# Kernel tuning notes

Measured on AMD Instinct MI355X. Metric: run time of the kernel, lower is better.

The kernel has to match this reference:

```python
import jax, jax.numpy as jnp
import numpy as np
import math

B, S, D, H, L = 4, 2048, 512, 8, 2
HD = D // H
NG = (3, 4, 5)
V = 30000          # n_gram_vocab_size
BASE = 31          # rolling hash base
NPATCH = 16
PLEN = S // NPATCH


def _ln(x, w, b, eps):
    m = x.mean(-1, keepdims=True)
    v = ((x - m) ** 2).mean(-1, keepdims=True)
    return (x - m) * jax.lax.rsqrt(v + eps) * w + b


def setup_inputs() -> dict:
    key = jax.random.key(0)
    ks = jax.random.split(key, 16)

    def nrm(i, shape, std=0.02):
        return jax.random.normal(ks[i], shape, dtype=jnp.float32) * std

    return {
        "byte_seq": jax.random.randint(ks[0], (B, S), 0, 256, dtype=jnp.int32),
        "patch_boundaries": jnp.arange(NPATCH + 1, dtype=jnp.int32) * PLEN,
        "byte_emb": nrm(1, (256, D), 1.0 / math.sqrt(D)),
        "ng_emb": nrm(2, (len(NG), V, D)),
        "tl_qkv_w": nrm(3, (L, 3 * D, D)),
        "tl_qkv_b": jnp.zeros((L, 3 * D), jnp.float32),
        "tl_out_w": nrm(4, (L, D, D)),
        "tl_out_b": jnp.zeros((L, D), jnp.float32),
        "tl_ln1_w": jnp.ones((L, D), jnp.float32),
        "tl_ln1_b": jnp.zeros((L, D), jnp.float32),
        "tl_ln2_w": jnp.ones((L, D), jnp.float32),
        "tl_ln2_b": jnp.zeros((L, D), jnp.float32),
        "tl_ff1_w": nrm(5, (L, 4 * D, D)),
        "tl_ff1_b": jnp.zeros((L, 4 * D), jnp.float32),
        "tl_ff2_w": nrm(6, (L, D, 4 * D)),
        "tl_ff2_b": jnp.zeros((L, D), jnp.float32),
        "ca_qkv_w": nrm(7, (3 * D, D)),
        "ca_qkv_b": jnp.zeros((3 * D,), jnp.float32),
        "ca_out_w": nrm(8, (D, D)),
        "ca_out_b": jnp.zeros((D,), jnp.float32),
        "ca_ln_w": jnp.ones((D,), jnp.float32),
        "ca_ln_b": jnp.zeros((D,), jnp.float32),
        "norm_w": jnp.ones((D,), jnp.float32),
        "norm_b": jnp.zeros((D,), jnp.float32),
    }


def _forward(byte_seq, patch_boundaries, byte_emb, ng_emb,
             tl_qkv_w, tl_qkv_b, tl_out_w, tl_out_b,
             tl_ln1_w, tl_ln1_b, tl_ln2_w, tl_ln2_b,
             tl_ff1_w, tl_ff1_b, tl_ff2_w, tl_ff2_b,
             ca_qkv_w, ca_qkv_b, ca_out_w, ca_out_b, ca_ln_w, ca_ln_b,
             norm_w, norm_b):
    x = byte_emb[byte_seq]                                  # [B,S,D]

    # n-gram rolling hash == polynomial hash mod V; computed in parallel
    # as windowed dot products with modular base powers (exact same values
    # as the sequential rolling-update loop in the torch code).
    ng_scale = 1.0 / (len(NG) + 1)
    for idx, n in enumerate(NG):
        powers = jnp.array([pow(BASE, n - 1 - i, V) for i in range(n)],
                           dtype=byte_seq.dtype)
        windows = jnp.stack([byte_seq[:, j:S - n + 1 + j] for j in range(n)],
                            axis=-1)                        # [B,S-n+1,n]
        h = (windows * powers).sum(-1) % V                   # [B,S-n+1]
        x = x.at[:, n - 1:].add(ng_emb[idx][h] * ng_scale)

    scale = 1.0 / math.sqrt(HD)
    neg = jnp.where(jnp.triu(jnp.ones((S, S), dtype=bool), 1),
                    -jnp.inf, 0.0).astype(x.dtype)           # causal additive mask

    # post-norm TransformerEncoderLayer (relu activation, dropout=0/eval)
    for l in range(L):
        qkv = x @ tl_qkv_w[l].T + tl_qkv_b[l]                # [B,S,3D]
        q, k, v = jnp.split(qkv, 3, axis=-1)
        q = q.reshape(B, S, H, HD).transpose(0, 2, 1, 3)
        k = k.reshape(B, S, H, HD).transpose(0, 2, 1, 3)
        v = v.reshape(B, S, H, HD).transpose(0, 2, 1, 3)
        scores = jnp.einsum('bhqd,bhkd->bhqk', q, k) * scale + neg
        a = jax.nn.softmax(scores, axis=-1)
        o = jnp.einsum('bhqk,bhkd->bhqd', a, v).transpose(0, 2, 1, 3).reshape(B, S, D)
        o = o @ tl_out_w[l].T + tl_out_b[l]
        x = _ln(x + o, tl_ln1_w[l], tl_ln1_b[l], 1e-5)
        ff = jax.nn.relu(x @ tl_ff1_w[l].T + tl_ff1_b[l]) @ tl_ff2_w[l].T + tl_ff2_b[l]
        x = _ln(x + ff, tl_ln2_w[l], tl_ln2_b[l], 1e-5)

    # uniform patch boundaries -> vectorized patch cross-attention
    npatch = patch_boundaries.shape[0] - 1
    plen = S // npatch
    xp = x.reshape(B, npatch, plen, D)
    query = xp.mean(axis=2)                                  # [B,P,D]
    qn = _ln(query, ca_ln_w, ca_ln_b, 1e-6)
    kvn = _ln(xp, ca_ln_w, ca_ln_b, 1e-6)
    wq, wk, wv = jnp.split(ca_qkv_w, 3, axis=0)
    bq, bk, bv = jnp.split(ca_qkv_b, 3)
    q = (qn @ wq.T + bq).reshape(B, npatch, H, HD)
    k = (kvn @ wk.T + bk).reshape(B, npatch, plen, H, HD)
    v = (kvn @ wv.T + bv).reshape(B, npatch, plen, H, HD)
    s = jnp.einsum('bphd,bplhd->bphl', q, k) * scale
    a = jax.nn.softmax(s, axis=-1)
    o = jnp.einsum('bphl,bplhd->bphd', a, v).reshape(B, npatch, D)
    patches = query + (o @ ca_out_w.T + ca_out_b)

    return _ln(x, norm_w, norm_b, 1e-6), _ln(patches, norm_w, norm_b, 1e-6)


def reference(byte_seq, patch_boundaries, byte_emb, ng_emb,
              tl_qkv_w, tl_qkv_b, tl_out_w, tl_out_b,
              tl_ln1_w, tl_ln1_b, tl_ln2_w, tl_ln2_b,
              tl_ff1_w, tl_ff1_b, tl_ff2_w, tl_ff2_b,
              ca_qkv_w, ca_qkv_b, ca_out_w, ca_out_b, ca_ln_w, ca_ln_b,
              norm_w, norm_b):
    return _forward(byte_seq, patch_boundaries, byte_emb, ng_emb,
                    tl_qkv_w, tl_qkv_b, tl_out_w, tl_out_b,
                    tl_ln1_w, tl_ln1_b, tl_ln2_w, tl_ln2_b,
                    tl_ff1_w, tl_ff1_b, tl_ff2_w, tl_ff2_b,
                    ca_qkv_w, ca_qkv_b, ca_out_w, ca_out_b, ca_ln_w, ca_ln_b,
                    norm_w, norm_b)
```

## Files before the change

kernel.cpp:

```cpp
#include <hip/hip_runtime.h>
#include <hip/hip_bf16.h>

#define B_ 4
#define S_ 2048
#define D_ 512
#define H_ 8
#define HD_ 64
#define L_ 2
#define V_ 30000
#define NPATCH_ 16
#define PLEN_ 128

typedef short bf16x8 __attribute__((ext_vector_type(8)));
typedef float f32x4 __attribute__((ext_vector_type(4)));

__device__ __forceinline__ unsigned short f2bf(float f) {
    unsigned u = __float_as_uint(f);
    return (unsigned short)((u + 0x7FFFu + ((u >> 16) & 1u)) >> 16);
}
__device__ __forceinline__ float bf2f(unsigned short u) {
    return __uint_as_float(((unsigned int)u) << 16);
}

#define C0_ (2*1536*512/4)
#define C1_ (2*512*512/4)
#define C2_ (2*2048*512/4)
#define C3_ (2*512*2048/4)
#define C4_ (1024*512/4)
__global__ __launch_bounds__(256) void cast5_kernel(
    const float* __restrict__ s0, const float* __restrict__ s1,
    const float* __restrict__ s2, const float* __restrict__ s3,
    const float* __restrict__ s4,
    unsigned short* __restrict__ d0, unsigned short* __restrict__ d1,
    unsigned short* __restrict__ d2, unsigned short* __restrict__ d3,
    unsigned short* __restrict__ d4)
{
    int i = blockIdx.x * 256 + threadIdx.x;
    const float* s; unsigned short* d;
    if      (i < C0_)                  { s = s0; d = d0; }
    else if ((i -= C0_) < C1_)         { s = s1; d = d1; }
    else if ((i -= C1_) < C2_)         { s = s2; d = d2; }
    else if ((i -= C2_) < C3_)         { s = s3; d = d3; }
    else if ((i -= C3_) < C4_)         { s = s4; d = d4; }
    else return;
    const float4 v = *reinterpret_cast<const float4*>(s + (size_t)i * 4);
    ushort4 o;
    o.x = f2bf(v.x); o.y = f2bf(v.y); o.z = f2bf(v.z); o.w = f2bf(v.w);
    *reinterpret_cast<ushort4*>(d + (size_t)i * 4) = o;
}

__global__ __launch_bounds__(128) void embed_ngram_kernel(
    const int* __restrict__ bytes, const float* __restrict__ byte_emb,
    const float* __restrict__ ng_emb, float* __restrict__ x,
    unsigned short* __restrict__ xb)
{
    const int bs = blockIdx.x;
    const int s  = bs % S_;
    const int b  = bs / S_;
    const int d  = threadIdx.x * 4;
    const int* brow = bytes + (size_t)b * S_;

    const int c = brow[s];
    float4 v = *reinterpret_cast<const float4*>(byte_emb + (size_t)c * D_ + d);

    if (s >= 2) {
        int h = (brow[s-2]*961 + brow[s-1]*31 + brow[s]) % V_;
        const float4 g = *reinterpret_cast<const float4*>(ng_emb + ((size_t)0*V_ + h)*D_ + d);
        v.x += 0.25f*g.x; v.y += 0.25f*g.y; v.z += 0.25f*g.z; v.w += 0.25f*g.w;
    }
    if (s >= 3) {
        int h = (brow[s-3]*29791 + brow[s-2]*961 + brow[s-1]*31 + brow[s]) % V_;
        const float4 g = *reinterpret_cast<const float4*>(ng_emb + ((size_t)1*V_ + h)*D_ + d);
        v.x += 0.25f*g.x; v.y += 0.25f*g.y; v.z += 0.25f*g.z; v.w += 0.25f*g.w;
    }
    if (s >= 4) {
        int h = (brow[s-4]*23521 + brow[s-3]*29791 + brow[s-2]*961 + brow[s-1]*31 + brow[s]) % V_;
        const float4 g = *reinterpret_cast<const float4*>(ng_emb + ((size_t)2*V_ + h)*D_ + d);
        v.x += 0.25f*g.x; v.y += 0.25f*g.y; v.z += 0.25f*g.z; v.w += 0.25f*g.w;
    }
    *reinterpret_cast<float4*>(x + (size_t)bs * D_ + d) = v;
    ushort4 o;
    o.x = f2bf(v.x); o.y = f2bf(v.y); o.z = f2bf(v.z); o.w = f2bf(v.w);
    *reinterpret_cast<ushort4*>(xb + (size_t)bs * D_ + d) = o;
}

template<int DO_RELU, int BF16OUT, int BN, int VT, int RESID>
__global__ __launch_bounds__(256) void mgemm_kernel(
    const unsigned short* __restrict__ Xb, const unsigned short* __restrict__ Wb,
    const float* __restrict__ bias, void* __restrict__ Yout,
    unsigned short* __restrict__ vtb, const float* __restrict__ resid,
    int M, int N, int K)
{
    constexpr int NT  = BN / 32;
    constexpr int NLB = BN / 32;
    __shared__ unsigned short As[128*64];
    __shared__ unsigned short Bs[BN*64];

    const int t    = threadIdx.x;
    const int lane = t & 63;
    const int w    = t >> 6;

    const int nwg = gridDim.x * gridDim.y;
    const int bid = blockIdx.y * gridDim.x + blockIdx.x;
    const int swz = (bid & 7) * (nwg >> 3) + (bid >> 3);
    const int bx  = swz % gridDim.x, by = swz / gridDim.x;

    const int bm   = by * 128, bn = bx * BN;
    const int l15  = lane & 15, lg = lane >> 4;
    const int wr   = w >> 1, wc = w & 1;

    int srow[4], scol[4];
#pragma unroll
    for (int i = 0; i < 4; ++i) {
        const int off = w*1024 + i*4096 + lane*16;
        srow[i] = off >> 7;
        scol[i] = ((off >> 4) & 7) ^ (srow[i] & 7);
    }

    f32x4 acc[4][NT];
#pragma unroll
    for (int mt = 0; mt < 4; ++mt)
#pragma unroll
        for (int nt = 0; nt < NT; ++nt) acc[mt][nt] = (f32x4){0.f,0.f,0.f,0.f};

    for (int kt = 0; kt < K; kt += 64) {
#pragma unroll
        for (int i = 0; i < 4; ++i) {
            const unsigned short* gA = Xb + (size_t)(bm + srow[i]) * K + kt + scol[i]*8;
            __builtin_amdgcn_global_load_lds(
                (const __attribute__((address_space(1))) void*)gA,
                (__attribute__((address_space(3))) void*)&As[w*512 + i*2048], 16, 0, 0);
        }
#pragma unroll
        for (int i = 0; i < NLB; ++i) {
            const unsigned short* gB = Wb + (size_t)(bn + srow[i]) * K + kt + scol[i]*8;
            __builtin_amdgcn_global_load_lds(
                (const __attribute__((address_space(1))) void*)gB,
                (__attribute__((address_space(3))) void*)&Bs[w*512 + i*2048], 16, 0, 0);
        }
        __syncthreads();

#pragma unroll
        for (int ks = 0; ks < 2; ++ks) {
            const int c16 = (ks*4 + lg) ^ (l15 & 7);
            bf16x8 a[4], b[NT];
#pragma unroll
            for (int mt = 0; mt < 4; ++mt)
                a[mt] = *reinterpret_cast<const bf16x8*>(&As[(wr*64 + mt*16 + l15)*64 + c16*8]);
#pragma unroll
            for (int nt = 0; nt < NT; ++nt)
                b[nt] = *reinterpret_cast<const bf16x8*>(&Bs[(wc*(BN/2) + nt*16 + l15)*64 + c16*8]);
#pragma unroll
            for (int mt = 0; mt < 4; ++mt)
#pragma unroll
                for (int nt = 0; nt < NT; ++nt)
                    acc[mt][nt] = __builtin_amdgcn_mfma_f32_16x16x32_bf16(
                        a[mt], b[nt], acc[mt][nt], 0, 0, 0);
        }
        __syncthreads();
    }

    float bv[NT];
#pragma unroll
    for (int nt = 0; nt < NT; ++nt) bv[nt] = bias[bn + wc*(BN/2) + nt*16 + l15];

#pragma unroll
    for (int mt = 0; mt < 4; ++mt) {
#pragma unroll
        for (int nt = 0; nt < NT; ++nt) {
            const int n = bn + wc*(BN/2) + nt*16 + l15;
#pragma unroll
            for (int r = 0; r < 4; ++r) {
                const int m = bm + wr*64 + mt*16 + 4*lg + r;
                float v = acc[mt][nt][r] + bv[nt];
                if (DO_RELU) v = fmaxf(v, 0.f);
                if (RESID) v += resid[(size_t)m * N + n];
                if constexpr (VT) {
                    if (n < 1024)
                        ((unsigned short*)Yout)[(size_t)m * 1024 + n] = f2bf(v);
                    else
                        vtb[((size_t)(m >> 11) * 512 + (n - 1024)) * 2048 + (m & 2047)] = f2bf(v);
                } else if constexpr (BF16OUT) {
                    ((unsigned short*)Yout)[(size_t)m * N + n] = f2bf(v);
                } else {
                    ((float*)Yout)[(size_t)m * N + n] = v;
                }
            }
        }
    }
}

__global__ __launch_bounds__(256) void attn_mfma_kernel(
    const unsigned short* __restrict__ qkvb, const unsigned short* __restrict__ vtb,
    unsigned short* __restrict__ ob)
{
    __shared__ unsigned short Ks[128*72];
    __shared__ unsigned short Vt[64*136];
    __shared__ unsigned short Plds[4*16*136];

    const int t    = threadIdx.x;
    const int lane = t & 63;
    const int w    = t >> 6;
    const int qp   = blockIdx.x;
    const int bh   = blockIdx.y;
    const int h    = bh & 7;
    const int b    = bh >> 3;

    const unsigned short* base = qkvb + (size_t)b * S_ * 1024;
    const int l15 = lane & 15, lg = lane >> 4;
    const int skey = t >> 1;
    const int sd0  = (t & 1) * 32;
    const int sdv  = t >> 2;
    const int skc  = (t & 3) * 32;
    const unsigned short* vbase = vtb + ((size_t)b * 512 + h*64 + sdv) * 2048;
    unsigned short* pw_base = Plds + w*16*136;
    const int pxor = ((l15 >> 3) & 1) << 1;

    bf16x8 kr0, kr1, kr2, kr3, vr0, vr1, vr2, vr3;
#define LOADREG(KT) { \
        const unsigned short* pk_ = base + (size_t)((KT) + skey) * 1024 + 512 + h*64 + sd0; \
        kr0 = *reinterpret_cast<const bf16x8*>(pk_);       \
        kr1 = *reinterpret_cast<const bf16x8*>(pk_ + 8);   \
        kr2 = *reinterpret_cast<const bf16x8*>(pk_ + 16);  \
        kr3 = *reinterpret_cast<const bf16x8*>(pk_ + 24);  \
        const unsigned short* pv_ = vbase + (KT) + skc;    \
        vr0 = *reinterpret_cast<const bf16x8*>(pv_);       \
        vr1 = *reinterpret_cast<const bf16x8*>(pv_ + 8);   \
        vr2 = *reinterpret_cast<const bf16x8*>(pv_ + 16);  \
        vr3 = *reinterpret_cast<const bf16x8*>(pv_ + 24); }

    LOADREG(0);

#pragma unroll
    for (int half = 0; half < 2; ++half) {
        const int qb  = half ? (31 - qp) : qp;
        const int q0w = qb * 64 + w * 16;

        bf16x8 qf0, qf1;
        {
            const unsigned short* qr = base + (size_t)(q0w + l15) * 1024 + h*64 + lg*8;
            qf0 = *reinterpret_cast<const bf16x8*>(qr);
            qf1 = *reinterpret_cast<const bf16x8*>(qr + 32);
        }

        f32x4 oacc[4];
#pragma unroll
        for (int i = 0; i < 4; ++i) oacc[i] = (f32x4){0.f,0.f,0.f,0.f};
        float mrow[4] = {-INFINITY,-INFINITY,-INFINITY,-INFINITY};
        float lrow[4] = {0.f,0.f,0.f,0.f};

        const int ntiles = (qb + 2) >> 1;
        for (int tile = 0; tile < ntiles; ++tile) {
            const int kt = tile * 128;
            __syncthreads();
            *reinterpret_cast<bf16x8*>(&Ks[skey*72 + sd0])      = kr0;
            *reinterpret_cast<bf16x8*>(&Ks[skey*72 + sd0 + 8])  = kr1;
            *reinterpret_cast<bf16x8*>(&Ks[skey*72 + sd0 + 16]) = kr2;
            *reinterpret_cast<bf16x8*>(&Ks[skey*72 + sd0 + 24]) = kr3;
            *reinterpret_cast<bf16x8*>(&Vt[sdv*136 + skc])      = vr0;
            *reinterpret_cast<bf16x8*>(&Vt[sdv*136 + skc + 8])  = vr1;
            *reinterpret_cast<bf16x8*>(&Vt[sdv*136 + skc + 16]) = vr2;
            *reinterpret_cast<bf16x8*>(&Vt[sdv*136 + skc + 24]) = vr3;
            __syncthreads();
            const int nkt = (tile + 1 < ntiles) ? (kt + 128) : 0;
            LOADREG(nkt);

            f32x4 sacc[8];
            __builtin_amdgcn_s_setprio(1);
#pragma unroll
            for (int kt16 = 0; kt16 < 8; ++kt16) {
                sacc[kt16] = (f32x4){0.f,0.f,0.f,0.f};
                const unsigned short* kp = &Ks[(kt16*16 + l15)*72 + lg*8];
                bf16x8 k0 = *reinterpret_cast<const bf16x8*>(kp);
                bf16x8 k1 = *reinterpret_cast<const bf16x8*>(kp + 32);
                sacc[kt16] = __builtin_amdgcn_mfma_f32_16x16x32_bf16(qf0, k0, sacc[kt16], 0, 0, 0);
                sacc[kt16] = __builtin_amdgcn_mfma_f32_16x16x32_bf16(qf1, k1, sacc[kt16], 0, 0, 0);
            }
            __builtin_amdgcn_s_setprio(0);

            const bool diag = (tile == ntiles - 1);
#pragma unroll
            for (int kt16 = 0; kt16 < 8; ++kt16) {
#pragma unroll
                for (int r = 0; r < 4; ++r) {
                    float s = sacc[kt16][r] * 0.125f;
                    if (diag) {
                        const int key = kt + kt16*16 + l15;
                        const int q   = q0w + 4*lg + r;
                        if (key > q) s = -INFINITY;
                    }
                    sacc[kt16][r] = s;
                }
            }
#pragma unroll
            for (int r = 0; r < 4; ++r) {
                float tm = fmaxf(
                    fmaxf(fmaxf(sacc[0][r], sacc[1][r]), fmaxf(sacc[2][r], sacc[3][r])),
                    fmaxf(fmaxf(sacc[4][r], sacc[5][r]), fmaxf(sacc[6][r], sacc[7][r])));
#pragma unroll
                for (int off = 8; off; off >>= 1) tm = fmaxf(tm, __shfl_xor(tm, off, 64));
                const float nm = fmaxf(mrow[r], tm);
                const float al = __expf(mrow[r] - nm);
                mrow[r] = nm;
                float ps = 0.f;
                const int prow = (4*lg + r)*136;
                const int cswz = ((lg & 2) << 3);
#pragma unroll
                for (int kt16 = 0; kt16 < 8; ++kt16) {
                    const float p = __expf(sacc[kt16][r] - nm);
                    ps += p;
                    pw_base[prow + ((kt16*16 + l15) ^ cswz)] = f2bf(p);
                }
#pragma unroll
                for (int off = 8; off; off >>= 1) ps += __shfl_xor(ps, off, 64);
                lrow[r] = lrow[r]*al + ps;
#pragma unroll
                for (int dt = 0; dt < 4; ++dt) oacc[dt][r] *= al;
            }

            const unsigned short* pr = &pw_base[l15*136];
            bf16x8 pa0 = *reinterpret_cast<const bf16x8*>(&pr[(( 0 + lg) ^ pxor)*8]);
            bf16x8 pa1 = *reinterpret_cast<const bf16x8*>(&pr[(( 4 + lg) ^ pxor)*8]);
            bf16x8 pa2 = *reinterpret_cast<const bf16x8*>(&pr[(( 8 + lg) ^ pxor)*8]);
            bf16x8 pa3 = *reinterpret_cast<const bf16x8*>(&pr[((12 + lg) ^ pxor)*8]);
            __builtin_amdgcn_s_setprio(1);
#pragma unroll
            for (int dt = 0; dt < 4; ++dt) {
                const unsigned short* vrow = &Vt[(dt*16 + l15)*136];
                bf16x8 v0 = *reinterpret_cast<const bf16x8*>(&vrow[( 0 + lg)*8]);
                bf16x8 v1 = *reinterpret_cast<const bf16x8*>(&vrow[( 4 + lg)*8]);
                bf16x8 v2 = *reinterpret_cast<const bf16x8*>(&vrow[( 8 + lg)*8]);
                bf16x8 v3 = *reinterpret_cast<const bf16x8*>(&vrow[(12 + lg)*8]);
                oacc[dt] = __builtin_amdgcn_mfma_f32_16x16x32_bf16(pa0, v0, oacc[dt], 0, 0, 0);
                oacc[dt] = __builtin_amdgcn_mfma_f32_16x16x32_bf16(pa1, v1, oacc[dt], 0, 0, 0);
                oacc[dt] = __builtin_amdgcn_mfma_f32_16x16x32_bf16(pa2, v2, oacc[dt], 0, 0, 0);
                oacc[dt] = __builtin_amdgcn_mfma_f32_16x16x32_bf16(pa3, v3, oacc[dt], 0, 0, 0);
            }
            __builtin_amdgcn_s_setprio(0);
        }

#pragma unroll
        for (int dt = 0; dt < 4; ++dt) {
#pragma unroll
            for (int r = 0; r < 4; ++r) {
                const int q = q0w + 4*lg + r;
                ob[((size_t)b*S_ + q)*D_ + h*64 + dt*16 + l15] = f2bf(oacc[dt][r] / lrow[r]);
            }
        }
    }
#undef LOADREG
}

__global__ __launch_bounds__(256) void ln_kernel(
    float* __restrict__ dst, unsigned short* __restrict__ dst2,
    const float* __restrict__ src, const float* __restrict__ add,
    const float* __restrict__ w, const float* __restrict__ b, float eps)
{
    const int row = blockIdx.x, tid = threadIdx.x;
    const int lane = tid & 63, wave = tid >> 6;
    float2 v = *reinterpret_cast<const float2*>(src + (size_t)row * D_ + tid*2);
    if (add) {
        float2 a = *reinterpret_cast<const float2*>(add + (size_t)row * D_ + tid*2);
        v.x += a.x; v.y += a.y;
    }
    __shared__ float red[8];
    float s = v.x + v.y;
#pragma unroll
    for (int off = 32; off; off >>= 1) s += __shfl_xor(s, off, 64);
    if (lane == 0) red[wave] = s;
    __syncthreads();
    const float mean = (red[0]+red[1]+red[2]+red[3]) * (1.f/D_);
    const float d0 = v.x - mean, d1 = v.y - mean;
    float sq = d0*d0 + d1*d1;
#pragma unroll
    for (int off = 32; off; off >>= 1) sq += __shfl_xor(sq, off, 64);
    if (lane == 0) red[4+wave] = sq;
    __syncthreads();
    const float var = (red[4]+red[5]+red[6]+red[7]) * (1.f/D_);
    const float inv = rsqrtf(var + eps);
    const float o0 = d0*inv*w[tid*2] + b[tid*2];
    const float o1 = d1*inv*w[tid*2+1] + b[tid*2+1];
    if (dst)
        *reinterpret_cast<float2*>(dst + (size_t)row * D_ + tid*2) = make_float2(o0, o1);
    if (dst2) {
        ushort2 u; u.x = f2bf(o0); u.y = f2bf(o1);
        *reinterpret_cast<ushort2*>(dst2 + (size_t)row * D_ + tid*2) = u;
    }
}

__global__ __launch_bounds__(256) void patch_tail_kernel(
    const float* __restrict__ x, const float* __restrict__ kvf,
    const float* __restrict__ ca_qkv_w, const float* __restrict__ ca_qkv_b,
    const float* __restrict__ ca_out_w, const float* __restrict__ ca_out_b,
    const float* __restrict__ ca_ln_w, const float* __restrict__ ca_ln_b,
    const float* __restrict__ norm_w, const float* __restrict__ norm_b,
    float* __restrict__ out)
{
    __shared__ float query[512];
    __shared__ float qs[512];
    __shared__ float ps[8*128];
    __shared__ float os[512];
    __shared__ float red[64];
    __shared__ float mred[8], sred[8];

    const int t  = threadIdx.x;
    const int bp = blockIdx.x;
    const int d0 = t * 2;
    const int lane = t & 63, wave = t >> 6;

    {
        const float* base = x + (size_t)bp * PLEN_ * D_ + d0;
        float s0 = 0.f, s1 = 0.f;
        for (int l = 0; l < PLEN_; ++l) {
            float2 v = *reinterpret_cast<const float2*>(base + (size_t)l * D_);
            s0 += v.x; s1 += v.y;
        }
        query[d0] = s0 * (1.f/PLEN_);
        query[d0+1] = s1 * (1.f/PLEN_);
    }
    __syncthreads();

    float qv0 = query[d0], qv1 = query[d0+1];
    {
        float s = qv0 + qv1;
#pragma unroll
        for (int off = 32; off; off >>= 1) s += __shfl_xor(s, off, 64);
        if (lane == 0) red[wave] = s;
        __syncthreads();
        const float mean = (red[0]+red[1]+red[2]+red[3]) * (1.f/D_);
        const float e0 = qv0 - mean, e1 = qv1 - mean;
        float sq = e0*e0 + e1*e1;
#pragma unroll
        for (int off = 32; off; off >>= 1) sq += __shfl_xor(sq, off, 64);
        if (lane == 0) red[4+wave] = sq;
        __syncthreads();
        const float var = (red[4]+red[5]+red[6]+red[7]) * (1.f/D_);
        const float inv = rsqrtf(var + 1e-6f);
        qs[d0]   = e0*inv*ca_ln_w[d0]   + ca_ln_b[d0];
        qs[d0+1] = e1*inv*ca_ln_w[d0+1] + ca_ln_b[d0+1];
    }
    __syncthreads();

    float qp0, qp1;
    {
        const float* w0 = ca_qkv_w + (size_t)d0 * D_;
        float a0 = ca_qkv_b[d0], a1 = ca_qkv_b[d0+1];
        for (int e = 0; e < D_; e += 4) {
            const float4 qn4 = *reinterpret_cast<const float4*>(&qs[e]);
            const float4 wa = *reinterpret_cast<const float4*>(w0 + e);
            const float4 wb = *reinterpret_cast<const float4*>(w0 + D_ + e);
            a0 += qn4.x*wa.x + qn4.y*wa.y + qn4.z*wa.z + qn4.w*wa.w;
            a1 += qn4.x*wb.x + qn4.y*wb.y + qn4.z*wb.z + qn4.w*wb.w;
        }
        qp0 = a0 * 0.125f; qp1 = a1 * 0.125f;
    }
    __syncthreads();
    qs[d0] = qp0; qs[d0+1] = qp1;
    __syncthreads();

    {
        const int h = t >> 5, c = t & 31;
        const float* qh = &qs[h*64];
#pragma unroll
        for (int j = 0; j < 4; ++j) {
            const int l = c*4 + j;
            const float* krow = kvf + ((size_t)bp*PLEN_ + l)*1024 + h*64;
            float acc = 0.f;
            for (int e = 0; e < 64; e += 4) {
                const float4 qe = *reinterpret_cast<const float4*>(qh + e);
                const float4 ke = *reinterpret_cast<const float4*>(krow + e);
                acc += qe.x*ke.x + qe.y*ke.y + qe.z*ke.z + qe.w*ke.w;
            }
            ps[h*128 + l] = acc;
        }
    }
    __syncthreads();

    {
        const int h = t >> 5, c = t & 31;
        float m4 = fmaxf(fmaxf(ps[h*128+c*4], ps[h*128+c*4+1]),
                         fmaxf(ps[h*128+c*4+2], ps[h*128+c*4+3]));
        red[h*8 + (c>>2)] = 0.f;
        __syncthreads();
        float mt_ = m4;
#pragma unroll
        for (int off = 1; off < 4; off <<= 1) mt_ = fmaxf(mt_, __shfl_xor(mt_, off, 64));
        if ((c & 3) == 0) red[h*8 + (c>>2)] = mt_;
        __syncthreads();
        if (t < 8) {
            float m = red[t*8];
#pragma unroll
            for (int j = 1; j < 8; ++j) m = fmaxf(m, red[t*8+j]);
            mred[t] = m;
        }
        __syncthreads();
        const float mh = mred[h];
        float ssum = 0.f;
#pragma unroll
        for (int j = 0; j < 4; ++j) {
            const float p = __expf(ps[h*128 + c*4 + j] - mh);
            ps[h*128 + c*4 + j] = p;
            ssum += p;
        }
#pragma unroll
        for (int off = 1; off < 4; off <<= 1) ssum += __shfl_xor(ssum, off, 64);
        if ((c & 3) == 0) red[h*8 + (c>>2)] = ssum;
        __syncthreads();
        if (t < 8) {
            float s = 0.f;
#pragma unroll
            for (int j = 0; j < 8; ++j) s += red[t*8+j];
            sred[t] = 1.f / s;
        }
    }
    __syncthreads();

    {
        const int h = t >> 5;
        const float* vbase = kvf + (size_t)bp*PLEN_*1024 + 512 + d0;
        float a0 = 0.f, a1 = 0.f;
        const float* ph = &ps[h*128];
        for (int l = 0; l < PLEN_; ++l) {
            const float p = ph[l];
            const float2 vv = *reinterpret_cast<const float2*>(vbase + (size_t)l*1024);
            a0 += p * vv.x; a1 += p * vv.y;
        }
        os[d0]   = a0 * sred[h];
        os[d0+1] = a1 * sred[h];
    }
    __syncthreads();

    float r0, r1;
    {
        const float* w0 = ca_out_w + (size_t)d0 * D_;
        float a0 = ca_out_b[d0], a1 = ca_out_b[d0+1];
        for (int e = 0; e < D_; e += 4) {
            const float4 oe = *reinterpret_cast<const float4*>(&os[e]);
            const float4 wa = *reinterpret_cast<const float4*>(w0 + e);
            const float4 wb = *reinterpret_cast<const float4*>(w0 + D_ + e);
            a0 += oe.x*wa.x + oe.y*wa.y + oe.z*wa.z + oe.w*wa.w;
            a1 += oe.x*wb.x + oe.y*wb.y + oe.z*wb.z + oe.w*wb.w;
        }
        r0 = query[d0] + a0;
        r1 = query[d0+1] + a1;
    }
    {
        float s = r0 + r1;
#pragma unroll
        for (int off = 32; off; off >>= 1) s += __shfl_xor(s, off, 64);
        __syncthreads();
        if (lane == 0) red[wave] = s;
        __syncthreads();
        const float mean = (red[0]+red[1]+red[2]+red[3]) * (1.f/D_);
        const float e0 = r0 - mean, e1 = r1 - mean;
        float sq = e0*e0 + e1*e1;
#pragma unroll
        for (int off = 32; off; off >>= 1) sq += __shfl_xor(sq, off, 64);
        if (lane == 0) red[4+wave] = sq;
        __syncthreads();
        const float var = (red[4]+red[5]+red[6]+red[7]) * (1.f/D_);
        const float inv = rsqrtf(var + 1e-6f);
        float* orow = out + ((size_t)(B_*S_) + bp) * D_;
        orow[d0]   = e0*inv*norm_w[d0]   + norm_b[d0];
        orow[d0+1] = e1*inv*norm_w[d0+1] + norm_b[d0+1];
    }
}

extern "C" void kernel_launch(void* const* d_in, const int* in_sizes, int n_in,
                              void* d_out, int out_size, void* d_ws, size_t ws_size,
                              hipStream_t stream)
{
    const int*   byte_seq = (const int*)d_in[0];
    const float* byte_emb = (const float*)d_in[2];
    const float* ng_emb   = (const float*)d_in[3];
    const float* qkv_w = (const float*)d_in[4];
    const float* qkv_b = (const float*)d_in[5];
    const float* out_w = (const float*)d_in[6];
    const float* out_b = (const float*)d_in[7];
    const float* ln1_w = (const float*)d_in[8];
    const float* ln1_b = (const float*)d_in[9];
    const float* ln2_w = (const float*)d_in[10];
    const float* ln2_b = (const float*)d_in[11];
    const float* ff1_w = (const float*)d_in[12];
    const float* ff1_b = (const float*)d_in[13];
    const float* ff2_w = (const float*)d_in[14];
    const float* ff2_b = (const float*)d_in[15];
    const float* ca_qkv_w = (const float*)d_in[16];
    const float* ca_qkv_b = (const float*)d_in[17];
    const float* ca_out_w = (const float*)d_in[18];
    const float* ca_out_b = (const float*)d_in[19];
    const float* ca_ln_w  = (const float*)d_in[20];
    const float* ca_ln_b  = (const float*)d_in[21];
    const float* norm_w   = (const float*)d_in[22];
    const float* norm_b   = (const float*)d_in[23];
    float* out = (float*)d_out;

    char* ws = (char*)d_ws;
    const size_t MB = 1024*1024;
    float*          x     = (float*)(ws);
    char*           bufA  = ws + 16*MB;
    float*          bufB  = (float*)(ws + 48*MB);
    unsigned short* vtb   = (unsigned short*)(ws + 48*MB);
    unsigned short* ob    = (unsigned short*)(ws + 64*MB);
    unsigned short* xb    = (unsigned short*)(ws + 72*MB);
    unsigned short* qkvw_b = (unsigned short*)(ws + 80*MB);
    unsigned short* outw_b = (unsigned short*)(ws + 83*MB);
    unsigned short* ff1w_b = (unsigned short*)(ws + 84*MB);
    unsigned short* ff2w_b = (unsigned short*)(ws + 88*MB);
    unsigned short* kvw_b  = (unsigned short*)(ws + 92*MB);

    unsigned short* qkvb = (unsigned short*)bufA;
    unsigned short* ff1b = (unsigned short*)bufA;
    float*          kvf  = (float*)bufA;

    const int M = B_ * S_;

    cast5_kernel<<<(C0_+C1_+C2_+C3_+C4_+255)/256, 256, 0, stream>>>(
        qkv_w, out_w, ff1_w, ff2_w, ca_qkv_w + 512*512,
        qkvw_b, outw_b, ff1w_b, ff2w_b, kvw_b);

    embed_ngram_kernel<<<M, 128, 0, stream>>>(byte_seq, byte_emb, ng_emb, x, xb);

    for (int l = 0; l < L_; ++l) {
        mgemm_kernel<0,1,128,1,0><<<dim3(1536/128, M/128), 256, 0, stream>>>(
            xb, qkvw_b + (size_t)l*1536*D_, qkv_b + l*1536, qkvb, vtb, nullptr, M, 1536, D_);
        attn_mfma_kernel<<<dim3(S_/128, B_*H_), 256, 0, stream>>>(qkvb, vtb, ob);
        mgemm_kernel<0,0,64,0,1><<<dim3(D_/64, M/128), 256, 0, stream>>>(
            ob, outw_b + (size_t)l*D_*D_, out_b + l*D_, bufB, nullptr, x, M, D_, D_);
        ln_kernel<<<M, 256, 0, stream>>>(x, xb, bufB, nullptr, ln1_w + l*D_, ln1_b + l*D_, 1e-5f);
        mgemm_kernel<1,1,128,0,0><<<dim3(2048/128, M/128), 256, 0, stream>>>(
            xb, ff1w_b + (size_t)l*2048*D_, ff1_b + l*2048, ff1b, nullptr, nullptr, M, 2048, D_);
        mgemm_kernel<0,0,64,0,1><<<dim3(D_/64, M/128), 256, 0, stream>>>(
            ff1b, ff2w_b + (size_t)l*D_*2048, ff2_b + l*D_, bufB, nullptr, x, M, D_, 2048);
        ln_kernel<<<M, 256, 0, stream>>>(x, xb, bufB, nullptr, ln2_w + l*D_, ln2_b + l*D_, 1e-5f);
    }

    ln_kernel<<<M, 256, 0, stream>>>(nullptr, xb, x, nullptr, ca_ln_w, ca_ln_b, 1e-6f);
    mgemm_kernel<0,0,128,0,0><<<dim3(1024/128, M/128), 256, 0, stream>>>(
        xb, kvw_b, ca_qkv_b + 512, kvf, nullptr, nullptr, M, 1024, D_);
    patch_tail_kernel<<<B_*NPATCH_, 256, 0, stream>>>(
        x, kvf, ca_qkv_w, ca_qkv_b, ca_out_w, ca_out_b,
        ca_ln_w, ca_ln_b, norm_w, norm_b, out);

    ln_kernel<<<M, 256, 0, stream>>>(out, nullptr, x, nullptr, norm_w, norm_b, 1e-6f);
}
```

Baseline: 511.1 us.

## Split causal attention into 64-row blocks and fuse final layernorms

The attention kernel drops the paired-half causal balancing, where one block handled query blocks qp and 31-qp with 128-key tiles. Each block now handles a single 64-query block with 64-key tiles, uses a smaller LDS footprint, and declares an occupancy hint in launch bounds. The grid is reordered so batch-head is the fast dimension. Separately, the cross-attention layernorm and the final output layernorm over the same input are fused into one kernel, saving one launch and one pass over x. The trade-off is uneven per-block work and more, smaller tiles, which means more syncs per key processed.

```diff
diff --git a/kernel.cpp b/kernel.cpp
--- a/kernel.cpp
+++ b/kernel.cpp
@@ -190,162 +190,139 @@
     }
 }
 
-__global__ __launch_bounds__(256) void attn_mfma_kernel(
+__global__ __launch_bounds__(256, 4) void attn_mfma_kernel(
     const unsigned short* __restrict__ qkvb, const unsigned short* __restrict__ vtb,
     unsigned short* __restrict__ ob)
 {
-    __shared__ unsigned short Ks[128*72];
-    __shared__ unsigned short Vt[64*136];
-    __shared__ unsigned short Plds[4*16*136];
+    __shared__ unsigned short Ks[64*72];
+    __shared__ unsigned short Vt[64*72];
+    __shared__ unsigned short Plds[4*16*72];
 
     const int t    = threadIdx.x;
     const int lane = t & 63;
     const int w    = t >> 6;
-    const int qp   = blockIdx.x;
-    const int bh   = blockIdx.y;
+    const int bh   = blockIdx.x;
+    const int qb   = blockIdx.y;
     const int h    = bh & 7;
     const int b    = bh >> 3;
+    const int q0w  = qb * 64 + w * 16;
 
     const unsigned short* base = qkvb + (size_t)b * S_ * 1024;
     const int l15 = lane & 15, lg = lane >> 4;
-    const int skey = t >> 1;
-    const int sd0  = (t & 1) * 32;
-    const int sdv  = t >> 2;
-    const int skc  = (t & 3) * 32;
-    const unsigned short* vbase = vtb + ((size_t)b * 512 + h*64 + sdv) * 2048;
-    unsigned short* pw_base = Plds + w*16*136;
+    const int skey = t >> 2;
+    const int sdk  = (t & 3) * 16;
+    const unsigned short* vbase = vtb + ((size_t)b * 512 + h*64 + skey) * 2048;
+    unsigned short* pw_base = Plds + w*16*72;
     const int pxor = ((l15 >> 3) & 1) << 1;
 
-    bf16x8 kr0, kr1, kr2, kr3, vr0, vr1, vr2, vr3;
+    bf16x8 kr0, kr1, vr0, vr1;
 #define LOADREG(KT) { \
-        const unsigned short* pk_ = base + (size_t)((KT) + skey) * 1024 + 512 + h*64 + sd0; \
+        const unsigned short* pk_ = base + (size_t)((KT) + skey) * 1024 + 512 + h*64 + sdk; \
         kr0 = *reinterpret_cast<const bf16x8*>(pk_);       \
         kr1 = *reinterpret_cast<const bf16x8*>(pk_ + 8);   \
-        kr2 = *reinterpret_cast<const bf16x8*>(pk_ + 16);  \
-        kr3 = *reinterpret_cast<const bf16x8*>(pk_ + 24);  \
-        const unsigned short* pv_ = vbase + (KT) + skc;    \
+        const unsigned short* pv_ = vbase + (KT) + sdk;    \
         vr0 = *reinterpret_cast<const bf16x8*>(pv_);       \
-        vr1 = *reinterpret_cast<const bf16x8*>(pv_ + 8);   \
-        vr2 = *reinterpret_cast<const bf16x8*>(pv_ + 16);  \
-        vr3 = *reinterpret_cast<const bf16x8*>(pv_ + 24); }
-
+        vr1 = *reinterpret_cast<const bf16x8*>(pv_ + 8); }
+
+    bf16x8 qf0, qf1;
+    {
+        const unsigned short* qr = base + (size_t)(q0w + l15) * 1024 + h*64 + lg*8;
+        qf0 = *reinterpret_cast<const bf16x8*>(qr);
+        qf1 = *reinterpret_cast<const bf16x8*>(qr + 32);
+    }
+
+    f32x4 oacc[4];
+#pragma unroll
+    for (int i = 0; i < 4; ++i) oacc[i] = (f32x4){0.f,0.f,0.f,0.f};
+    float mrow[4] = {-INFINITY,-INFINITY,-INFINITY,-INFINITY};
+    float lrow[4] = {0.f,0.f,0.f,0.f};
+
+    const int ntiles = qb + 1;
     LOADREG(0);
 
-#pragma unroll
-    for (int half = 0; half < 2; ++half) {
-        const int qb  = half ? (31 - qp) : qp;
-        const int q0w = qb * 64 + w * 16;
-
-        bf16x8 qf0, qf1;
-        {
-            const unsigned short* qr = base + (size_t)(q0w + l15) * 1024 + h*64 + lg*8;
-            qf0 = *reinterpret_cast<const bf16x8*>(qr);
-            qf1 = *reinterpret_cast<const bf16x8*>(qr + 32);
-        }
-
-        f32x4 oacc[4];
-#pragma unroll
-        for (int i = 0; i < 4; ++i) oacc[i] = (f32x4){0.f,0.f,0.f,0.f};
-        float mrow[4] = {-INFINITY,-INFINITY,-INFINITY,-INFINITY};
-        float lrow[4] = {0.f,0.f,0.f,0.f};
-
-        const int ntiles = (qb + 2) >> 1;
-        for (int tile = 0; tile < ntiles; ++tile) {
-            const int kt = tile * 128;
-            __syncthreads();
-            *reinterpret_cast<bf16x8*>(&Ks[skey*72 + sd0])      = kr0;
-            *reinterpret_cast<bf16x8*>(&Ks[skey*72 + sd0 + 8])  = kr1;
-            *reinterpret_cast<bf16x8*>(&Ks[skey*72 + sd0 + 16]) = kr2;
-            *reinterpret_cast<bf16x8*>(&Ks[skey*72 + sd0 + 24]) = kr3;
-            *reinterpret_cast<bf16x8*>(&Vt[sdv*136 + skc])      = vr0;
-            *reinterpret_cast<bf16x8*>(&Vt[sdv*136 + skc + 8])  = vr1;
-            *reinterpret_cast<bf16x8*>(&Vt[sdv*136 + skc + 16]) = vr2;
-            *reinterpret_cast<bf16x8*>(&Vt[sdv*136 + skc + 24]) = vr3;
-            __syncthreads();
-            const int nkt = (tile + 1 < ntiles) ? (kt + 128) : 0;
-            LOADREG(nkt);
-
-            f32x4 sacc[8];
-            __builtin_amdgcn_s_setprio(1);
-#pragma unroll
-            for (int kt16 = 0; kt16 < 8; ++kt16) {
-                sacc[kt16] = (f32x4){0.f,0.f,0.f,0.f};
-                const unsigned short* kp = &Ks[(kt16*16 + l15)*72 + lg*8];
-                bf16x8 k0 = *reinterpret_cast<const bf16x8*>(kp);
-                bf16x8 k1 = *reinterpret_cast<const bf16x8*>(kp + 32);
-                sacc[kt16] = __builtin_amdgcn_mfma_f32_16x16x32_bf16(qf0, k0, sacc[kt16], 0, 0, 0);
-                sacc[kt16] = __builtin_amdgcn_mfma_f32_16x16x32_bf16(qf1, k1, sacc[kt16], 0, 0, 0);
+    for (int tile = 0; tile < ntiles; ++tile) {
+        const int kt = tile * 64;
+        __syncthreads();
+        *reinterpret_cast<bf16x8*>(&Ks[skey*72 + sdk])     = kr0;
+        *reinterpret_cast<bf16x8*>(&Ks[skey*72 + sdk + 8]) = kr1;
+        *reinterpret_cast<bf16x8*>(&Vt[skey*72 + sdk])     = vr0;
+        *reinterpret_cast<bf16x8*>(&Vt[skey*72 + sdk + 8]) = vr1;
+        __syncthreads();
+        const int nkt = (tile + 1 < ntiles) ? (kt + 64) : 0;
+        LOADREG(nkt);
+
+        f32x4 sacc[4];
+        __builtin_amdgcn_s_setprio(1);
+#pragma unroll
+        for (int kt16 = 0; kt16 < 4; ++kt16) {
+            sacc[kt16] = (f32x4){0.f,0.f,0.f,0.f};
+            const unsigned short* kp = &Ks[(kt16*16 + l15)*72 + lg*8];
+            bf16x8 k0 = *reinterpret_cast<const bf16x8*>(kp);
+            bf16x8 k1 = *reinterpret_cast<const bf16x8*>(kp + 32);
+            sacc[kt16] = __builtin_amdgcn_mfma_f32_16x16x32_bf16(qf0, k0, sacc[kt16], 0, 0, 0);
+            sacc[kt16] = __builtin_amdgcn_mfma_f32_16x16x32_bf16(qf1, k1, sacc[kt16], 0, 0, 0);
+        }
+        __builtin_amdgcn_s_setprio(0);
+
+        const bool diag = (tile == ntiles - 1);
+#pragma unroll
+        for (int kt16 = 0; kt16 < 4; ++kt16) {
+#pragma unroll
+            for (int r = 0; r < 4; ++r) {
+                float sv = sacc[kt16][r] * 0.125f;
+                if (diag) {
+                    const int key = kt + kt16*16 + l15;
+                    const int q   = q0w + 4*lg + r;
+                    if (key > q) sv = -INFINITY;
+                }
+                sacc[kt16][r] = sv;
             }
-            __builtin_amdgcn_s_setprio(0);
-
-            const bool diag = (tile == ntiles - 1);
-#pragma unroll
-            for (int kt16 = 0; kt16 < 8; ++kt16) {
-#pragma unroll
-                for (int r = 0; r < 4; ++r) {
-                    float s = sacc[kt16][r] * 0.125f;
-                    if (diag) {
-                        const int key = kt + kt16*16 + l15;
-                        const int q   = q0w + 4*lg + r;
-                        if (key > q) s = -INFINITY;
-                    }
-                    sacc[kt16][r] = s;
-                }
+        }
+#pragma unroll
+        for (int r = 0; r < 4; ++r) {
+            float tm = fmaxf(fmaxf(sacc[0][r], sacc[1][r]), fmaxf(sacc[2][r], sacc[3][r]));
+#pragma unroll
+            for (int off = 8; off; off >>= 1) tm = fmaxf(tm, __shfl_xor(tm, off, 64));
+            const float nm = fmaxf(mrow[r], tm);
+            const float al = __expf(mrow[r] - nm);
+            mrow[r] = nm;
+            float ps = 0.f;
+            const int prow = (4*lg + r)*72;
+            const int cswz = ((lg & 2) << 3);
+#pragma unroll
+            for (int kt16 = 0; kt16 < 4; ++kt16) {
+                const float p = __expf(sacc[kt16][r] - nm);
+                ps += p;
+                pw_base[prow + ((kt16*16 + l15) ^ cswz)] = f2bf(p);
             }
 #pragma unroll
-            for (int r = 0; r < 4; ++r) {
-                float tm = fmaxf(
-                    fmaxf(fmaxf(sacc[0][r], sacc[1][r]), fmaxf(sacc[2][r], sacc[3][r])),
-                    fmaxf(fmaxf(sacc[4][r], sacc[5][r]), fmaxf(sacc[6][r], sacc[7][r])));
-#pragma unroll
-                for (int off = 8; off; off >>= 1) tm = fmaxf(tm, __shfl_xor(tm, off, 64));
-                const float nm = fmaxf(mrow[r], tm);
-                const float al = __expf(mrow[r] - nm);
-                mrow[r] = nm;
-                float ps = 0.f;
-                const int prow = (4*lg + r)*136;
-                const int cswz = ((lg & 2) << 3);
-#pragma unroll
-                for (int kt16 = 0; kt16 < 8; ++kt16) {
-                    const float p = __expf(sacc[kt16][r] - nm);
-                    ps += p;
-                    pw_base[prow + ((kt16*16 + l15) ^ cswz)] = f2bf(p);
-                }
-#pragma unroll
-                for (int off = 8; off; off >>= 1) ps += __shfl_xor(ps, off, 64);
-                lrow[r] = lrow[r]*al + ps;
-#pragma unroll
-                for (int dt = 0; dt < 4; ++dt) oacc[dt][r] *= al;
-            }
-
-            const unsigned short* pr = &pw_base[l15*136];
-            bf16x8 pa0 = *reinterpret_cast<const bf16x8*>(&pr[(( 0 + lg) ^ pxor)*8]);
-            bf16x8 pa1 = *reinterpret_cast<const bf16x8*>(&pr[(( 4 + lg) ^ pxor)*8]);
-            bf16x8 pa2 = *reinterpret_cast<const bf16x8*>(&pr[(( 8 + lg) ^ pxor)*8]);
-            bf16x8 pa3 = *reinterpret_cast<const bf16x8*>(&pr[((12 + lg) ^ pxor)*8]);
-            __builtin_amdgcn_s_setprio(1);
-#pragma unroll
-            for (int dt = 0; dt < 4; ++dt) {
-                const unsigned short* vrow = &Vt[(dt*16 + l15)*136];
-                bf16x8 v0 = *reinterpret_cast<const bf16x8*>(&vrow[( 0 + lg)*8]);
-                bf16x8 v1 = *reinterpret_cast<const bf16x8*>(&vrow[( 4 + lg)*8]);
-                bf16x8 v2 = *reinterpret_cast<const bf16x8*>(&vrow[( 8 + lg)*8]);
-                bf16x8 v3 = *reinterpret_cast<const bf16x8*>(&vrow[(12 + lg)*8]);
-                oacc[dt] = __builtin_amdgcn_mfma_f32_16x16x32_bf16(pa0, v0, oacc[dt], 0, 0, 0);
-                oacc[dt] = __builtin_amdgcn_mfma_f32_16x16x32_bf16(pa1, v1, oacc[dt], 0, 0, 0);
-                oacc[dt] = __builtin_amdgcn_mfma_f32_16x16x32_bf16(pa2, v2, oacc[dt], 0, 0, 0);
-                oacc[dt] = __builtin_amdgcn_mfma_f32_16x16x32_bf16(pa3, v3, oacc[dt], 0, 0, 0);
-            }
-            __builtin_amdgcn_s_setprio(0);
-        }
-
+            for (int off = 8; off; off >>= 1) ps += __shfl_xor(ps, off, 64);
+            lrow[r] = lrow[r]*al + ps;
+#pragma unroll
+            for (int dt = 0; dt < 4; ++dt) oacc[dt][r] *= al;
+        }
+
+        const unsigned short* pr = &pw_base[l15*72];
+        bf16x8 pa0 = *reinterpret_cast<const bf16x8*>(&pr[((0 + lg) ^ pxor)*8]);
+        bf16x8 pa1 = *reinterpret_cast<const bf16x8*>(&pr[((4 + lg) ^ pxor)*8]);
+        __builtin_amdgcn_s_setprio(1);
 #pragma unroll
         for (int dt = 0; dt < 4; ++dt) {
-#pragma unroll
-            for (int r = 0; r < 4; ++r) {
-                const int q = q0w + 4*lg + r;
-                ob[((size_t)b*S_ + q)*D_ + h*64 + dt*16 + l15] = f2bf(oacc[dt][r] / lrow[r]);
-            }
+            const unsigned short* vrow = &Vt[(dt*16 + l15)*72];
+            bf16x8 v0 = *reinterpret_cast<const bf16x8*>(&vrow[(0 + lg)*8]);
+            bf16x8 v1 = *reinterpret_cast<const bf16x8*>(&vrow[(4 + lg)*8]);
+            oacc[dt] = __builtin_amdgcn_mfma_f32_16x16x32_bf16(pa0, v0, oacc[dt], 0, 0, 0);
+            oacc[dt] = __builtin_amdgcn_mfma_f32_16x16x32_bf16(pa1, v1, oacc[dt], 0, 0, 0);
+        }
+        __builtin_amdgcn_s_setprio(0);
+    }
+
+#pragma unroll
+    for (int dt = 0; dt < 4; ++dt) {
+#pragma unroll
+        for (int r = 0; r < 4; ++r) {
+            const int q = q0w + 4*lg + r;
+            ob[((size_t)b*S_ + q)*D_ + h*64 + dt*16 + l15] = f2bf(oacc[dt][r] / lrow[r]);
         }
     }
 #undef LOADREG
@@ -386,6 +363,40 @@
         ushort2 u; u.x = f2bf(o0); u.y = f2bf(o1);
         *reinterpret_cast<ushort2*>(dst2 + (size_t)row * D_ + tid*2) = u;
     }
+}
+
+__global__ __launch_bounds__(256) void ln_dual_kernel(
+    float* __restrict__ out, unsigned short* __restrict__ kvnb,
+    const float* __restrict__ src,
+    const float* __restrict__ nw, const float* __restrict__ nb,
+    const float* __restrict__ cw, const float* __restrict__ cb)
+{
+    const int row = blockIdx.x, tid = threadIdx.x;
+    const int lane = tid & 63, wave = tid >> 6;
+    float2 v = *reinterpret_cast<const float2*>(src + (size_t)row * D_ + tid*2);
+    __shared__ float red[8];
+    float s = v.x + v.y;
+#pragma unroll
+    for (int off = 32; off; off >>= 1) s += __shfl_xor(s, off, 64);
+    if (lane == 0) red[wave] = s;
+    __syncthreads();
+    const float mean = (red[0]+red[1]+red[2]+red[3]) * (1.f/D_);
+    const float d0 = v.x - mean, d1 = v.y - mean;
+    float sq = d0*d0 + d1*d1;
+#pragma unroll
+    for (int off = 32; off; off >>= 1) sq += __shfl_xor(sq, off, 64);
+    if (lane == 0) red[4+wave] = sq;
+    __syncthreads();
+    const float var = (red[4]+red[5]+red[6]+red[7]) * (1.f/D_);
+    const float inv = rsqrtf(var + 1e-6f);
+    const float n0 = d0*inv;
+    const float n1 = d1*inv;
+    *reinterpret_cast<float2*>(out + (size_t)row * D_ + tid*2) =
+        make_float2(n0*nw[tid*2] + nb[tid*2], n1*nw[tid*2+1] + nb[tid*2+1]);
+    ushort2 u;
+    u.x = f2bf(n0*cw[tid*2]   + cb[tid*2]);
+    u.y = f2bf(n1*cw[tid*2+1] + cb[tid*2+1]);
+    *reinterpret_cast<ushort2*>(kvnb + (size_t)row * D_ + tid*2) = u;
 }
 
 __global__ __launch_bounds__(256) void patch_tail_kernel(
@@ -624,7 +635,7 @@
     for (int l = 0; l < L_; ++l) {
         mgemm_kernel<0,1,128,1,0><<<dim3(1536/128, M/128), 256, 0, stream>>>(
             xb, qkvw_b + (size_t)l*1536*D_, qkv_b + l*1536, qkvb, vtb, nullptr, M, 1536, D_);
-        attn_mfma_kernel<<<dim3(S_/128, B_*H_), 256, 0, stream>>>(qkvb, vtb, ob);
+        attn_mfma_kernel<<<dim3(B_*H_, S_/64), 256, 0, stream>>>(qkvb, vtb, ob);
         mgemm_kernel<0,0,64,0,1><<<dim3(D_/64, M/128), 256, 0, stream>>>(
             ob, outw_b + (size_t)l*D_*D_, out_b + l*D_, bufB, nullptr, x, M, D_, D_);
         ln_kernel<<<M, 256, 0, stream>>>(x, xb, bufB, nullptr, ln1_w + l*D_, ln1_b + l*D_, 1e-5f);
@@ -635,12 +646,10 @@
         ln_kernel<<<M, 256, 0, stream>>>(x, xb, bufB, nullptr, ln2_w + l*D_, ln2_b + l*D_, 1e-5f);
     }
 
-    ln_kernel<<<M, 256, 0, stream>>>(nullptr, xb, x, nullptr, ca_ln_w, ca_ln_b, 1e-6f);
+    ln_dual_kernel<<<M, 256, 0, stream>>>(out, xb, x, norm_w, norm_b, ca_ln_w, ca_ln_b);
     mgemm_kernel<0,0,128,0,0><<<dim3(1024/128, M/128), 256, 0, stream>>>(
         xb, kvw_b, ca_qkv_b + 512, kvf, nullptr, nullptr, M, 1024, D_);
     patch_tail_kernel<<<B_*NPATCH_, 256, 0, stream>>>(
         x, kvf, ca_qkv_w, ca_qkv_b, ca_out_w, ca_out_b,
         ca_ln_w, ca_ln_b, norm_w, norm_b, out);
-
-    ln_kernel<<<M, 256, 0, stream>>>(out, nullptr, x, nullptr, norm_w, norm_b, 1e-6f);
-}
+}
```

After: 547.2 us. 7.1% more time.
